# Optimization experiments

Measured on AMD Instinct MI355X. Metric: run time of the kernel, lower is better.

## Reference

```python
import jax, jax.numpy as jnp
import numpy as np

EMB = 1024
HEADS = 16
DH = EMB // HEADS
EPS = 1e-5


def _layernorm(x, w, b):
    mean = jnp.mean(x, axis=-1, keepdims=True)
    var = jnp.mean((x - mean) ** 2, axis=-1, keepdims=True)  # unbiased=False
    return w * (x - mean) / jnp.sqrt(var + EPS) + b


def _gelu_tanh(x):
    c = jnp.sqrt(jnp.asarray(2.0 / jnp.pi, x.dtype))
    return 0.5 * x * (1.0 + jnp.tanh(c * (x + 0.044715 * x ** 3)))


def setup_inputs() -> dict:
    key = jax.random.key(0)
    ks = jax.random.split(key, 8)
    B, N = 2, 2048
    s = lambda fan_in: 1.0 / np.sqrt(fan_in)
    # weights stored as [in, out] (torch Linear applied as x @ W.T == x @ W_here)
    return {
        "x": jax.random.normal(ks[0], (B, N, EMB), jnp.float32),
        "ln1_w": jnp.ones((EMB,), jnp.float32),
        "ln1_b": jnp.zeros((EMB,), jnp.float32),
        "w_qkv": jax.random.normal(ks[1], (EMB, 3 * EMB), jnp.float32) * s(EMB),  # qkv_bias=False
        "w_attn_proj": jax.random.normal(ks[2], (EMB, EMB), jnp.float32) * s(EMB),
        "b_attn_proj": jnp.zeros((EMB,), jnp.float32),
        "ln2_w": jnp.ones((EMB,), jnp.float32),
        "ln2_b": jnp.zeros((EMB,), jnp.float32),
        "w_fc": jax.random.normal(ks[3], (EMB, 4 * EMB), jnp.float32) * s(EMB),
        "b_fc": jnp.zeros((4 * EMB,), jnp.float32),
        "w_proj": jax.random.normal(ks[4], (4 * EMB, EMB), jnp.float32) * s(4 * EMB),
        "b_proj": jnp.zeros((EMB,), jnp.float32),
    }


def reference(x, ln1_w, ln1_b, w_qkv, w_attn_proj, b_attn_proj,
              ln2_w, ln2_b, w_fc, b_fc, w_proj, b_proj):
    B, N, _ = x.shape
    # --- attention sublayer (pre-LN) ---
    h = _layernorm(x, ln1_w, ln1_b)
    qkv = h @ w_qkv  # [B,N,3E]
    q, k, v = jnp.split(qkv, 3, axis=-1)
    # [B,H,N,Dh]
    q = q.reshape(B, N, HEADS, DH).transpose(0, 2, 1, 3)
    k = k.reshape(B, N, HEADS, DH).transpose(0, 2, 1, 3)
    v = v.reshape(B, N, HEADS, DH).transpose(0, 2, 1, 3)
    scores = jnp.einsum("bhqd,bhkd->bhqk", q, k) * (DH ** -0.5)
    causal = jnp.tril(jnp.ones((N, N), bool))
    scores = jnp.where(causal, scores, -jnp.inf)
    attn = jax.nn.softmax(scores, axis=-1)  # attn_pdrop=0 (eval)
    ctx = jnp.einsum("bhqk,bhkd->bhqd", attn, v)
    ctx = ctx.transpose(0, 2, 1, 3).reshape(B, N, EMB)
    x = x + (ctx @ w_attn_proj + b_attn_proj)  # resid_pdrop=0
    # --- MLP sublayer (pre-LN) ---
    h = _layernorm(x, ln2_w, ln2_b)
    h = _gelu_tanh(h @ w_fc + b_fc)
    x = x + (h @ w_proj + b_proj)
    return x
```

## Files before the change

kernel.cpp:

```cpp
#include <hip/hip_runtime.h>
#include <stdint.h>

#define EMB 1024
#define NHEAD 16
#define DH 64
#define SEQ 2048
#define NTOK 4096

typedef __attribute__((ext_vector_type(8))) short s16x8;
typedef __attribute__((ext_vector_type(4))) short s16x4;
typedef __attribute__((ext_vector_type(4))) float f32x4;
typedef __attribute__((ext_vector_type(4))) unsigned short u16x4;

__device__ __forceinline__ unsigned short f2bf(float f){
    union { float f; unsigned int u; } v; v.f = f;
    unsigned int r = v.u + 0x7fffu + ((v.u >> 16) & 1u);
    return (unsigned short)(r >> 16);
}

__device__ __forceinline__ f32x4 mfma16(s16x8 a, s16x8 b, f32x4 c){
    return __builtin_amdgcn_mfma_f32_16x16x32_bf16(a, b, c, 0, 0, 0);
}

__device__ __forceinline__ void gload16(const void* g, void* l){
    __builtin_amdgcn_global_load_lds((const __attribute__((address_space(1))) void*)g,
                                     (__attribute__((address_space(3))) void*)l, 16, 0, 0);
}

__device__ __forceinline__ s16x8 cat8(s16x4 a, s16x4 b){
    s16x8 r;
    r[0]=a[0]; r[1]=a[1]; r[2]=a[2]; r[3]=a[3];
    r[4]=b[0]; r[5]=b[1]; r[6]=b[2]; r[7]=b[3];
    return r;
}

__device__ __forceinline__ unsigned cvtpk(float lo, float hi){
    unsigned r;
    asm("v_cvt_pk_bf16_f32 %0, %1, %2" : "=v"(r) : "v"(lo), "v"(hi));
    return r;
}

__device__ __forceinline__ s16x8 qscale(s16x8 q){
    s16x8 r;
    #pragma unroll
    for (int e = 0; e < 8; ++e){
        union { float f; unsigned u; } v;
        v.u = ((unsigned)(unsigned short)q[e]) << 16;
        v.f *= 0.125f;
        r[e] = (short)f2bf(v.f);
    }
    return r;
}

__global__ __launch_bounds__(256) void convT4_kernel(const float* __restrict__ q, unsigned short* __restrict__ qo,
                                                     const float* __restrict__ a, unsigned short* __restrict__ ao,
                                                     const float* __restrict__ f, unsigned short* __restrict__ fo,
                                                     const float* __restrict__ p, unsigned short* __restrict__ po){
    __shared__ float tile[32][33];
    int id = blockIdx.x;
    const float* in; unsigned short* out; int R, C, bx, by;
    if (id < 3072)      { in = q; out = qo; R = 1024; C = 3072; bx = id % 96;  by = id / 96;  }
    else if (id < 4096) { id -= 3072; in = a; out = ao; R = 1024; C = 1024; bx = id % 32; by = id / 32; }
    else if (id < 8192) { id -= 4096; in = f; out = fo; R = 1024; C = 4096; bx = id % 128; by = id / 128; }
    else                { id -= 8192; in = p; out = po; R = 4096; C = 1024; bx = id % 32; by = id / 32; }
    const int c0 = bx * 32, r0 = by * 32;
    const int tx = threadIdx.x, ty = threadIdx.y;
    #pragma unroll
    for (int k = 0; k < 4; ++k)
        tile[ty*4+k][tx] = in[(long)(r0 + ty*4 + k) * C + c0 + tx];
    __syncthreads();
    #pragma unroll
    for (int k = 0; k < 4; ++k)
        out[(long)(c0 + ty*4 + k) * R + r0 + tx] = f2bf(tile[tx][ty*4+k]);
}

__global__ __launch_bounds__(256) void vT_kernel(const unsigned short* __restrict__ qkv,
                                                 unsigned short* __restrict__ vtg){
    __shared__ unsigned short tile[64*64];
    const int bh = blockIdx.y, b = bh >> 4, h = bh & 15;
    const int n0 = blockIdx.x * 64;
    const int t = threadIdx.x;
    const int nr = t >> 3, c0 = (t & 7) * 8;
    #pragma unroll
    for (int hh = 0; hh < 2; ++hh){
        const int n = nr + hh*32;
        uint4 vv = *(const uint4*)&qkv[(long)(b*SEQ + n0 + n)*3072 + 2048 + h*64 + c0];
        *(uint4*)((char*)tile + n*128 + ((c0*2) ^ (((n>>3)&7)<<4))) = vv;
    }
    __syncthreads();
    #pragma unroll
    for (int hh = 0; hh < 2; ++hh){
        const int d = nr + hh*32;
        union { unsigned short u[8]; uint4 v; } tmp;
        #pragma unroll
        for (int j = 0; j < 8; ++j){
            const int n = c0 + j;
            tmp.u[j] = *(const unsigned short*)((char*)tile + n*128 + ((d*2) ^ (((n>>3)&7)<<4)));
        }
        *(uint4*)&vtg[((long)bh*64 + d)*2048 + n0 + c0] = tmp.v;
    }
}

__global__ __launch_bounds__(256) void ln_kernel(const float* __restrict__ x,
                                                 const float* __restrict__ w,
                                                 const float* __restrict__ b,
                                                 unsigned short* __restrict__ out){
    const int row = blockIdx.x, tid = threadIdx.x;
    const float4 v = ((const float4*)(x + (long)row * EMB))[tid];
    float s  = v.x + v.y + v.z + v.w;
    float ss = v.x*v.x + v.y*v.y + v.z*v.z + v.w*v.w;
    #pragma unroll
    for (int off = 32; off >= 1; off >>= 1){
        s  += __shfl_xor(s,  off, 64);
        ss += __shfl_xor(ss, off, 64);
    }
    __shared__ float ps[4], pss[4];
    const int wv = tid >> 6;
    if ((tid & 63) == 0){ ps[wv] = s; pss[wv] = ss; }
    __syncthreads();
    s  = ps[0] + ps[1] + ps[2] + ps[3];
    ss = pss[0] + pss[1] + pss[2] + pss[3];
    const float mean = s * (1.0f/EMB);
    const float var  = ss * (1.0f/EMB) - mean*mean;
    const float rstd = rsqrtf(var + 1e-5f);
    const float4 wv4 = ((const float4*)w)[tid];
    const float4 bv4 = ((const float4*)b)[tid];
    u16x4 o;
    o[0] = f2bf((v.x - mean) * rstd * wv4.x + bv4.x);
    o[1] = f2bf((v.y - mean) * rstd * wv4.y + bv4.y);
    o[2] = f2bf((v.z - mean) * rstd * wv4.z + bv4.z);
    o[3] = f2bf((v.w - mean) * rstd * wv4.w + bv4.w);
    *(u16x4*)(out + (long)row * EMB + tid * 4) = o;
}

template<int EPI>
__global__ __launch_bounds__(256, 2) void gemm4_kernel(const unsigned short* __restrict__ A,
                                                       const unsigned short* __restrict__ Bt,
                                                       const float* __restrict__ bias,
                                                       void* __restrict__ out0,
                                                       int M, int N, int K,
                                                       int xr, int yr){
    __shared__ unsigned short As[2][128*64];
    __shared__ unsigned short Bs[2][128*64];
    const int tid = threadIdx.x, lane = tid & 63, w = tid >> 6;
    const int lm = lane & 15, g = lane >> 4;
    const int wr = w >> 1, wc = w & 1;

    const int gx = gridDim.x;
    const int o = blockIdx.y * gx + blockIdx.x;
    const int x = o & 7, j = o >> 3;
    const int nrx = gx / xr;
    const int m0 = ((x / nrx) * yr + j / xr) * 128;
    const int n0 = ((x % nrx) * xr + j % xr) * 128;
    const int nkt = K / 64;

    const int r8 = tid >> 3;
    const int src = (((tid & 7) * 16) ^ ((r8 & 7) << 4)) >> 1;
    char* AsB = (char*)&As[0][0];
    char* BsB = (char*)&Bs[0][0];

    auto stage = [&](int bu, int kt){
        #pragma unroll
        for (int p = 0; p < 4; ++p)
            gload16(&A[(long)(m0 + p*32 + r8) * K + kt + src], AsB + bu*16384 + p*4096 + tid*16);
        #pragma unroll
        for (int p = 0; p < 4; ++p)
            gload16(&Bt[(long)(n0 + p*32 + r8) * K + kt + src], BsB + bu*16384 + p*4096 + tid*16);
    };

    f32x4 zero = {0.0f, 0.0f, 0.0f, 0.0f};
    f32x4 acc[4][4];
    #pragma unroll
    for (int i = 0; i < 4; ++i)
        #pragma unroll
        for (int jj = 0; jj < 4; ++jj) acc[i][jj] = zero;

    stage(0, 0);
    int cur = 0;
    const int axor = (lm & 7) << 4;
    for (int t = 0; t < nkt; ++t){
        if (t + 1 < nkt){
            stage(cur ^ 1, (t + 1) * 64);
            asm volatile("s_waitcnt vmcnt(8)" ::: "memory");
        } else {
            asm volatile("s_waitcnt vmcnt(0)" ::: "memory");
        }
        __builtin_amdgcn_s_barrier();
        asm volatile("" ::: "memory");
        const char* Ab = AsB + cur*16384;
        const char* Bb = BsB + cur*16384;
        #pragma unroll
        for (int kk = 0; kk < 2; ++kk){
            s16x8 af[4], bf[4];
            #pragma unroll
            for (int i = 0; i < 4; ++i)
                af[i] = *(const s16x8*)(Ab + (wr*64 + i*16 + lm)*128 + ((kk*64 + g*16) ^ axor));
            #pragma unroll
            for (int jj = 0; jj < 4; ++jj)
                bf[jj] = *(const s16x8*)(Bb + (wc*64 + jj*16 + lm)*128 + ((kk*64 + g*16) ^ axor));
            asm volatile("s_waitcnt lgkmcnt(0)" ::: "memory");
            __builtin_amdgcn_sched_barrier(0);
            __builtin_amdgcn_s_setprio(1);
            #pragma unroll
            for (int i = 0; i < 4; ++i)
                #pragma unroll
                for (int jj = 0; jj < 4; ++jj)
                    acc[i][jj] = mfma16(bf[jj], af[i], acc[i][jj]);
            __builtin_amdgcn_s_setprio(0);
        }
        asm volatile("" ::: "memory");
        __builtin_amdgcn_s_barrier();
        asm volatile("" ::: "memory");
        cur ^= 1;
    }

    #pragma unroll
    for (int i = 0; i < 4; ++i){
        const int row = m0 + wr*64 + i*16 + lm;
        #pragma unroll
        for (int jj = 0; jj < 4; ++jj){
            const int col = n0 + wc*64 + jj*16 + 4*g;
            const f32x4 v = acc[i][jj];
            if (EPI == 0){
                u16x4 ov;
                ov[0] = f2bf(v[0]); ov[1] = f2bf(v[1]);
                ov[2] = f2bf(v[2]); ov[3] = f2bf(v[3]);
                *(u16x4*)&((unsigned short*)out0)[(long)row * N + col] = ov;
            } else {
                u16x4 ov;
                #pragma unroll
                for (int r = 0; r < 4; ++r){
                    const float xx = v[r] + bias[col + r];
                    const float z = 0.7978845608f * (xx + 0.044715f * xx * xx * xx);
                    ov[r] = f2bf(xx / (1.0f + __expf(-2.0f * z)));
                }
                *(u16x4*)&((unsigned short*)out0)[(long)row * N + col] = ov;
            }
        }
    }
}

__global__ __launch_bounds__(256, 3) void gemm5_kernel(const unsigned short* __restrict__ A,
                                                       const unsigned short* __restrict__ Bt,
                                                       const float* __restrict__ bias,
                                                       const float* __restrict__ resid,
                                                       float* __restrict__ out0,
                                                       int M, int N, int K,
                                                       int xr, int yr){
    __shared__ unsigned short As[2][128*64];
    __shared__ unsigned short Bs[2][64*64];
    const int tid = threadIdx.x, lane = tid & 63, w = tid >> 6;
    const int lm = lane & 15, g = lane >> 4;
    const int wr = w >> 1, wc = w & 1;

    const int gx = gridDim.x;
    const int o = blockIdx.y * gx + blockIdx.x;
    const int x = o & 7, j = o >> 3;
    const int nrx = gx / xr;
    const int m0 = ((x / nrx) * yr + j / xr) * 128;
    const int n0 = ((x % nrx) * xr + j % xr) * 64;
    const int nkt = K / 64;

    const int r8 = tid >> 3;
    const int src = (((tid & 7) * 16) ^ ((r8 & 7) << 4)) >> 1;
    char* AsB = (char*)&As[0][0];
    char* BsB = (char*)&Bs[0][0];

    auto stage = [&](int bu, int kt){
        #pragma unroll
        for (int p = 0; p < 4; ++p)
            gload16(&A[(long)(m0 + p*32 + r8) * K + kt + src], AsB + bu*16384 + p*4096 + tid*16);
        #pragma unroll
        for (int p = 0; p < 2; ++p)
            gload16(&Bt[(long)(n0 + p*32 + r8) * K + kt + src], BsB + bu*8192 + p*4096 + tid*16);
    };

    f32x4 zero = {0.0f, 0.0f, 0.0f, 0.0f};
    f32x4 acc[4][2];
    #pragma unroll
    for (int i = 0; i < 4; ++i)
        #pragma unroll
        for (int jj = 0; jj < 2; ++jj) acc[i][jj] = zero;

    stage(0, 0);
    int cur = 0;
    const int axor = (lm & 7) << 4;
    for (int t = 0; t < nkt; ++t){
        if (t + 1 < nkt){
            stage(cur ^ 1, (t + 1) * 64);
            asm volatile("s_waitcnt vmcnt(6)" ::: "memory");
        } else {
            asm volatile("s_waitcnt vmcnt(0)" ::: "memory");
        }
        __builtin_amdgcn_s_barrier();
        asm volatile("" ::: "memory");
        const char* Ab = AsB + cur*16384;
        const char* Bb = BsB + cur*8192;
        #pragma unroll
        for (int kk = 0; kk < 2; ++kk){
            s16x8 af[4], bf[2];
            #pragma unroll
            for (int i = 0; i < 4; ++i)
                af[i] = *(const s16x8*)(Ab + (wr*64 + i*16 + lm)*128 + ((kk*64 + g*16) ^ axor));
            #pragma unroll
            for (int jj = 0; jj < 2; ++jj)
                bf[jj] = *(const s16x8*)(Bb + (wc*32 + jj*16 + lm)*128 + ((kk*64 + g*16) ^ axor));
            asm volatile("s_waitcnt lgkmcnt(0)" ::: "memory");
            __builtin_amdgcn_sched_barrier(0);
            __builtin_amdgcn_s_setprio(1);
            #pragma unroll
            for (int i = 0; i < 4; ++i)
                #pragma unroll
                for (int jj = 0; jj < 2; ++jj)
                    acc[i][jj] = mfma16(bf[jj], af[i], acc[i][jj]);
            __builtin_amdgcn_s_setprio(0);
        }
        asm volatile("" ::: "memory");
        __builtin_amdgcn_s_barrier();
        asm volatile("" ::: "memory");
        cur ^= 1;
    }

    #pragma unroll
    for (int i = 0; i < 4; ++i){
        const int row = m0 + wr*64 + i*16 + lm;
        #pragma unroll
        for (int jj = 0; jj < 2; ++jj){
            const int col = n0 + wc*32 + jj*16 + 4*g;
            const f32x4 v = acc[i][jj];
            const float4 bb = *(const float4*)&bias[col];
            const float4 rr = *(const float4*)&resid[(long)row * N + col];
            float4 ov;
            ov.x = v[0] + bb.x + rr.x;
            ov.y = v[1] + bb.y + rr.y;
            ov.z = v[2] + bb.z + rr.z;
            ov.w = v[3] + bb.w + rr.w;
            *(float4*)&out0[(long)row * N + col] = ov;
        }
    }
}

__global__ __launch_bounds__(256) void attn_kernel(const unsigned short* __restrict__ qkv,
                                                   const unsigned short* __restrict__ vtg,
                                                   unsigned short* __restrict__ ctx){
    __shared__ unsigned short Ks[3][4096];
    __shared__ unsigned short Vs[3][4096];
    int id0 = blockIdx.y * 16 + blockIdx.x;
    const int id = (id0 & 7) * 64 + (id0 >> 3);
    const int pair = id & 15, bh = id >> 4;
    const int b = bh >> 4, h = bh & 15;
    const int tid = threadIdx.x, lane = tid & 63, w = tid >> 6;
    const int lm = lane & 15, g = lane >> 4;
    const long qkvb = (long)b * SEQ * 3072;
    const unsigned short* kglob = qkv + qkvb + 1024 + h*64;
    const unsigned short* vglob = vtg + (long)bh * 64 * 2048;

    const int srow = tid >> 3;
    const int soff = (tid & 7) * 16;
    const int swz = (lm & 7) << 4;
    f32x4 zero = {0.0f, 0.0f, 0.0f, 0.0f};

    #pragma unroll 1
    for (int grp = 0; grp < 2; ++grp){
        const int qg = (grp == 0) ? pair : (31 - pair);
        const int q0 = qg * 64;
        const int nt = qg + 1;
        const int qrow = q0 + w*16 + lm;

        const unsigned short* qrp = qkv + qkvb + (long)qrow*3072 + h*64;
        const s16x8 qf0 = qscale(*(const s16x8*)(qrp + g*8));
        const s16x8 qf1 = qscale(*(const s16x8*)(qrp + 32 + g*8));

        f32x4 o[4];
        #pragma unroll
        for (int d = 0; d < 4; ++d) o[d] = zero;
        float lsum = 0.0f;

        auto stageKV = [&](int t, int bu){
            const int kv0 = t * 64;
            #pragma unroll
            for (int hh = 0; hh < 2; ++hh){
                const int row = srow + hh*32;
                const int sw  = soff ^ ((row & 7) << 4);
                gload16(kglob + (long)(kv0 + row)*3072 + (sw >> 1),
                        (char*)&Ks[bu][0] + hh*4096 + w*1024);
                gload16(vglob + (long)row*2048 + kv0 + (sw >> 1),
                        (char*)&Vs[bu][0] + hh*4096 + w*1024);
            }
        };
        auto qkt = [&](int bu, f32x4* sc){
            const char* Kb = (const char*)&Ks[bu][0];
            #pragma unroll
            for (int s = 0; s < 4; ++s){
                const char* rp = Kb + (s*16 + lm)*128;
                s16x8 kf0 = *(const s16x8*)(rp + ((g*16) ^ swz));
                s16x8 kf1 = *(const s16x8*)(rp + ((64 + g*16) ^ swz));
                f32x4 a = mfma16(kf0, qf0, zero);
                sc[s] = mfma16(kf1, qf1, a);
            }
        };

        __builtin_amdgcn_s_barrier();
        asm volatile("" ::: "memory");
        stageKV(0, 0);
        if (nt > 1){
            stageKV(1, 1);
            asm volatile("s_waitcnt vmcnt(4)" ::: "memory");
        } else {
            asm volatile("s_waitcnt vmcnt(0)" ::: "memory");
        }
        __builtin_amdgcn_s_barrier();
        asm volatile("" ::: "memory");

        f32x4 sc[4], scN[4];
        qkt(0, sc);

        #pragma unroll 1
        for (int t = 0; t < nt; ++t){
            const bool more = (t + 1 < nt);
            if (more){
                asm volatile("s_waitcnt vmcnt(0)" ::: "memory");
                __builtin_amdgcn_s_barrier();
                asm volatile("" ::: "memory");
                if (t + 2 < nt) stageKV(t + 2, (t + 2) % 3);
                qkt((t + 1) % 3, scN);
            }

            if (t == nt - 1){
                #pragma unroll
                for (int s = 0; s < 4; ++s)
                    #pragma unroll
                    for (int r = 0; r < 4; ++r)
                        if (s*16 + 4*g + r > w*16 + lm) sc[s][r] = -1e30f;
            }
            float pp[4][4];
            #pragma unroll
            for (int s = 0; s < 4; ++s)
                #pragma unroll
                for (int r = 0; r < 4; ++r){
                    const float e = __expf(sc[s][r]);
                    pp[s][r] = e;
                    lsum += e;
                }

            union { unsigned u[4]; s16x8 v; } P0, P1;
            P0.u[0] = cvtpk(pp[0][0], pp[0][1]);
            P0.u[1] = cvtpk(pp[0][2], pp[0][3]);
            P0.u[2] = cvtpk(pp[1][0], pp[1][1]);
            P0.u[3] = cvtpk(pp[1][2], pp[1][3]);
            P1.u[0] = cvtpk(pp[2][0], pp[2][1]);
            P1.u[1] = cvtpk(pp[2][2], pp[2][3]);
            P1.u[2] = cvtpk(pp[3][0], pp[3][1]);
            P1.u[3] = cvtpk(pp[3][2], pp[3][3]);

            const char* Vb = (const char*)&Vs[t % 3][0];
            #pragma unroll
            for (int d = 0; d < 4; ++d){
                const char* vrp = Vb + (d*16 + lm)*128;
                s16x4 a0 = *(const s16x4*)(vrp + ((g*8) ^ swz));
                s16x4 a1 = *(const s16x4*)(vrp + ((32 + g*8) ^ swz));
                o[d] = mfma16(cat8(a0, a1), P0.v, o[d]);
                s16x4 b0 = *(const s16x4*)(vrp + ((64 + g*8) ^ swz));
                s16x4 b1 = *(const s16x4*)(vrp + ((96 + g*8) ^ swz));
                o[d] = mfma16(cat8(b0, b1), P1.v, o[d]);
            }
            if (more){
                #pragma unroll
                for (int s4 = 0; s4 < 4; ++s4) sc[s4] = scN[s4];
            }
        }

        lsum += __shfl_xor(lsum, 16, 64);
        lsum += __shfl_xor(lsum, 32, 64);
        const float inv = 1.0f / lsum;
        unsigned short* cw = ctx + (long)(b*SEQ + qrow)*EMB + h*DH + 4*g;
        #pragma unroll
        for (int d = 0; d < 4; ++d){
            u16x4 ov;
            ov[0] = f2bf(o[d][0]*inv); ov[1] = f2bf(o[d][1]*inv);
            ov[2] = f2bf(o[d][2]*inv); ov[3] = f2bf(o[d][3]*inv);
            *(u16x4*)(cw + d*16) = ov;
        }
    }
}

extern "C" void kernel_launch(void* const* d_in, const int* in_sizes, int n_in,
                              void* d_out, int out_size, void* d_ws, size_t ws_size,
                              hipStream_t stream){
    const float* x     = (const float*)d_in[0];
    const float* ln1_w = (const float*)d_in[1];
    const float* ln1_b = (const float*)d_in[2];
    const float* w_qkv = (const float*)d_in[3];
    const float* w_ap  = (const float*)d_in[4];
    const float* b_ap  = (const float*)d_in[5];
    const float* ln2_w = (const float*)d_in[6];
    const float* ln2_b = (const float*)d_in[7];
    const float* w_fc  = (const float*)d_in[8];
    const float* b_fc  = (const float*)d_in[9];
    const float* w_pr  = (const float*)d_in[10];
    const float* b_pr  = (const float*)d_in[11];
    float* out = (float*)d_out;

    char* ws = (char*)d_ws;
    unsigned short* wqkvT = (unsigned short*)(ws + 0);
    unsigned short* wapT  = (unsigned short*)(ws + 6291456);
    unsigned short* wfcT  = (unsigned short*)(ws + 8388608);
    unsigned short* wprT  = (unsigned short*)(ws + 16777216);
    unsigned short* h1    = (unsigned short*)(ws + 25165824);
    unsigned short* vtg   = (unsigned short*)(ws + 25165824);
    unsigned short* qkv   = (unsigned short*)(ws + 33554432);
    unsigned short* ctx   = (unsigned short*)(ws + 58720256);
    float*          x1    = (float*)(ws + 67108864);
    unsigned short* h2    = (unsigned short*)(ws + 83886080);
    unsigned short* afc   = (unsigned short*)(ws + 92274688);

    convT4_kernel<<<12288, dim3(32, 8, 1), 0, stream>>>(
        w_qkv, wqkvT, w_ap, wapT, w_fc, wfcT, w_pr, wprT);

    ln_kernel<<<NTOK, 256, 0, stream>>>(x, ln1_w, ln1_b, h1);

    gemm4_kernel<0><<<dim3(3072/128, NTOK/128), 256, 0, stream>>>(
        h1, wqkvT, nullptr, qkv, NTOK, 3072, 1024, 12, 8);

    vT_kernel<<<dim3(SEQ/64, 32), 256, 0, stream>>>(qkv, vtg);

    attn_kernel<<<dim3(16, 32), 256, 0, stream>>>(qkv, vtg, ctx);

    gemm5_kernel<<<dim3(1024/64, NTOK/128), 256, 0, stream>>>(
        ctx, wapT, b_ap, x, x1, NTOK, 1024, 1024, 8, 8);

    ln_kernel<<<NTOK, 256, 0, stream>>>(x1, ln2_w, ln2_b, h2);

    gemm4_kernel<2><<<dim3(4096/128, NTOK/128), 256, 0, stream>>>(
        h2, wfcT, b_fc, afc, NTOK, 4096, 1024, 16, 8);

    gemm5_kernel<<<dim3(1024/64, NTOK/128), 256, 0, stream>>>(
        afc, wprT, b_pr, x1, out, NTOK, 1024, 4096, 8, 8);
}
```

Baseline: 238.6 us.

## Replace block-tiled GEMMs with single-wave 64x64 tile GEMM kernel

Replaces the 256-thread, 128x128 and 128x64 tile GEMM kernels with one templated kernel in which a single 64-lane wavefront owns a 64x64 output tile, using a K-step of 32 and no block barriers. All four projection GEMMs now launch many small one-wave blocks, and the bias-plus-residual epilogue is folded into the same template. The intent is to remove barrier synchronisation and gain more resident waves and finer scheduling. In exchange, each wave re-reads A and B tiles with much less reuse, which raises global and L2 traffic per FLOP. It also drops the priority hints around the MFMA block.

```diff
diff --git a/kernel.cpp b/kernel.cpp
--- a/kernel.cpp
+++ b/kernel.cpp
@@ -134,38 +134,39 @@
 }
 
 template<int EPI>
-__global__ __launch_bounds__(256, 2) void gemm4_kernel(const unsigned short* __restrict__ A,
-                                                       const unsigned short* __restrict__ Bt,
-                                                       const float* __restrict__ bias,
-                                                       void* __restrict__ out0,
-                                                       int M, int N, int K,
-                                                       int xr, int yr){
-    __shared__ unsigned short As[2][128*64];
-    __shared__ unsigned short Bs[2][128*64];
-    const int tid = threadIdx.x, lane = tid & 63, w = tid >> 6;
+__global__ __launch_bounds__(64, 3) void gemm6_kernel(const unsigned short* __restrict__ A,
+                                                      const unsigned short* __restrict__ Bt,
+                                                      const float* __restrict__ bias,
+                                                      const float* __restrict__ resid,
+                                                      void* __restrict__ out0,
+                                                      int M, int N, int K,
+                                                      int xr, int yr){
+    __shared__ unsigned short As[2][2048];
+    __shared__ unsigned short Bs[2][2048];
+    const int lane = threadIdx.x;
     const int lm = lane & 15, g = lane >> 4;
-    const int wr = w >> 1, wc = w & 1;
-
-    const int gx = gridDim.x;
-    const int o = blockIdx.y * gx + blockIdx.x;
+
+    const int gx = N >> 6;
+    const int o = blockIdx.x;
     const int x = o & 7, j = o >> 3;
     const int nrx = gx / xr;
-    const int m0 = ((x / nrx) * yr + j / xr) * 128;
-    const int n0 = ((x % nrx) * xr + j % xr) * 128;
-    const int nkt = K / 64;
-
-    const int r8 = tid >> 3;
-    const int src = (((tid & 7) * 16) ^ ((r8 & 7) << 4)) >> 1;
-    char* AsB = (char*)&As[0][0];
-    char* BsB = (char*)&Bs[0][0];
+    const int m0 = ((x / nrx) * yr + j / xr) * 64;
+    const int n0 = ((x % nrx) * xr + j % xr) * 64;
+    const int nkt = K >> 5;
+
+    const int srow = lane >> 2;
+    const int srcoff = ((lane & 3) * 8) ^ ((srow & 3) << 3);
+    const unsigned short* Ab = A + (long)(m0 + srow) * K + srcoff;
+    const unsigned short* Bb = Bt + (long)(n0 + srow) * K + srcoff;
+    const long rstep = (long)16 * K;
 
     auto stage = [&](int bu, int kt){
         #pragma unroll
         for (int p = 0; p < 4; ++p)
-            gload16(&A[(long)(m0 + p*32 + r8) * K + kt + src], AsB + bu*16384 + p*4096 + tid*16);
+            gload16(Ab + p*rstep + kt, (char*)&As[bu][0] + p*1024 + lane*16);
         #pragma unroll
         for (int p = 0; p < 4; ++p)
-            gload16(&Bt[(long)(n0 + p*32 + r8) * K + kt + src], BsB + bu*16384 + p*4096 + tid*16);
+            gload16(Bb + p*rstep + kt, (char*)&Bs[bu][0] + p*1024 + lane*16);
     };
 
     f32x4 zero = {0.0f, 0.0f, 0.0f, 0.0f};
@@ -176,166 +177,64 @@
         for (int jj = 0; jj < 4; ++jj) acc[i][jj] = zero;
 
     stage(0, 0);
-    int cur = 0;
-    const int axor = (lm & 7) << 4;
+    const int rxor = (lm & 3) << 4;
     for (int t = 0; t < nkt; ++t){
         if (t + 1 < nkt){
-            stage(cur ^ 1, (t + 1) * 64);
+            stage((t + 1) & 1, (t + 1) * 32);
             asm volatile("s_waitcnt vmcnt(8)" ::: "memory");
         } else {
             asm volatile("s_waitcnt vmcnt(0)" ::: "memory");
         }
-        __builtin_amdgcn_s_barrier();
-        asm volatile("" ::: "memory");
-        const char* Ab = AsB + cur*16384;
-        const char* Bb = BsB + cur*16384;
-        #pragma unroll
-        for (int kk = 0; kk < 2; ++kk){
-            s16x8 af[4], bf[4];
-            #pragma unroll
-            for (int i = 0; i < 4; ++i)
-                af[i] = *(const s16x8*)(Ab + (wr*64 + i*16 + lm)*128 + ((kk*64 + g*16) ^ axor));
+        const char* Ap = (const char*)&As[t & 1][0];
+        const char* Bp = (const char*)&Bs[t & 1][0];
+        s16x8 af[4], bf[4];
+        #pragma unroll
+        for (int i = 0; i < 4; ++i)
+            af[i] = *(const s16x8*)(Ap + (i*16 + lm)*64 + ((g*16) ^ rxor));
+        #pragma unroll
+        for (int jj = 0; jj < 4; ++jj)
+            bf[jj] = *(const s16x8*)(Bp + (jj*16 + lm)*64 + ((g*16) ^ rxor));
+        asm volatile("s_waitcnt lgkmcnt(0)" ::: "memory");
+        __builtin_amdgcn_sched_barrier(0);
+        #pragma unroll
+        for (int i = 0; i < 4; ++i)
             #pragma unroll
             for (int jj = 0; jj < 4; ++jj)
-                bf[jj] = *(const s16x8*)(Bb + (wc*64 + jj*16 + lm)*128 + ((kk*64 + g*16) ^ axor));
-            asm volatile("s_waitcnt lgkmcnt(0)" ::: "memory");
-            __builtin_amdgcn_sched_barrier(0);
-            __builtin_amdgcn_s_setprio(1);
-            #pragma unroll
-            for (int i = 0; i < 4; ++i)
-                #pragma unroll
-                for (int jj = 0; jj < 4; ++jj)
-                    acc[i][jj] = mfma16(bf[jj], af[i], acc[i][jj]);
-            __builtin_amdgcn_s_setprio(0);
-        }
-        asm volatile("" ::: "memory");
-        __builtin_amdgcn_s_barrier();
-        asm volatile("" ::: "memory");
-        cur ^= 1;
+                acc[i][jj] = mfma16(bf[jj], af[i], acc[i][jj]);
     }
 
     #pragma unroll
     for (int i = 0; i < 4; ++i){
-        const int row = m0 + wr*64 + i*16 + lm;
+        const int row = m0 + i*16 + lm;
         #pragma unroll
         for (int jj = 0; jj < 4; ++jj){
-            const int col = n0 + wc*64 + jj*16 + 4*g;
+            const int col = n0 + jj*16 + 4*g;
             const f32x4 v = acc[i][jj];
             if (EPI == 0){
                 u16x4 ov;
                 ov[0] = f2bf(v[0]); ov[1] = f2bf(v[1]);
                 ov[2] = f2bf(v[2]); ov[3] = f2bf(v[3]);
                 *(u16x4*)&((unsigned short*)out0)[(long)row * N + col] = ov;
+            } else if (EPI == 1){
+                const float4 bb = *(const float4*)&bias[col];
+                const float4 rr = *(const float4*)&resid[(long)row * N + col];
+                float4 ov;
+                ov.x = v[0] + bb.x + rr.x;
+                ov.y = v[1] + bb.y + rr.y;
+                ov.z = v[2] + bb.z + rr.z;
+                ov.w = v[3] + bb.w + rr.w;
+                *(float4*)&((float*)out0)[(long)row * N + col] = ov;
             } else {
+                const float4 bb = *(const float4*)&bias[col];
                 u16x4 ov;
                 #pragma unroll
                 for (int r = 0; r < 4; ++r){
-                    const float xx = v[r] + bias[col + r];
+                    const float xx = v[r] + ((const float*)&bb)[r];
                     const float z = 0.7978845608f * (xx + 0.044715f * xx * xx * xx);
                     ov[r] = f2bf(xx / (1.0f + __expf(-2.0f * z)));
                 }
                 *(u16x4*)&((unsigned short*)out0)[(long)row * N + col] = ov;
             }
-        }
-    }
-}
-
-__global__ __launch_bounds__(256, 3) void gemm5_kernel(const unsigned short* __restrict__ A,
-                                                       const unsigned short* __restrict__ Bt,
-                                                       const float* __restrict__ bias,
-                                                       const float* __restrict__ resid,
-                                                       float* __restrict__ out0,
-                                                       int M, int N, int K,
-                                                       int xr, int yr){
-    __shared__ unsigned short As[2][128*64];
-    __shared__ unsigned short Bs[2][64*64];
-    const int tid = threadIdx.x, lane = tid & 63, w = tid >> 6;
-    const int lm = lane & 15, g = lane >> 4;
-    const int wr = w >> 1, wc = w & 1;
-
-    const int gx = gridDim.x;
-    const int o = blockIdx.y * gx + blockIdx.x;
-    const int x = o & 7, j = o >> 3;
-    const int nrx = gx / xr;
-    const int m0 = ((x / nrx) * yr + j / xr) * 128;
-    const int n0 = ((x % nrx) * xr + j % xr) * 64;
-    const int nkt = K / 64;
-
-    const int r8 = tid >> 3;
-    const int src = (((tid & 7) * 16) ^ ((r8 & 7) << 4)) >> 1;
-    char* AsB = (char*)&As[0][0];
-    char* BsB = (char*)&Bs[0][0];
-
-    auto stage = [&](int bu, int kt){
-        #pragma unroll
-        for (int p = 0; p < 4; ++p)
-            gload16(&A[(long)(m0 + p*32 + r8) * K + kt + src], AsB + bu*16384 + p*4096 + tid*16);
-        #pragma unroll
-        for (int p = 0; p < 2; ++p)
-            gload16(&Bt[(long)(n0 + p*32 + r8) * K + kt + src], BsB + bu*8192 + p*4096 + tid*16);
-    };
-
-    f32x4 zero = {0.0f, 0.0f, 0.0f, 0.0f};
-    f32x4 acc[4][2];
-    #pragma unroll
-    for (int i = 0; i < 4; ++i)
-        #pragma unroll
-        for (int jj = 0; jj < 2; ++jj) acc[i][jj] = zero;
-
-    stage(0, 0);
-    int cur = 0;
-    const int axor = (lm & 7) << 4;
-    for (int t = 0; t < nkt; ++t){
-        if (t + 1 < nkt){
-            stage(cur ^ 1, (t + 1) * 64);
-            asm volatile("s_waitcnt vmcnt(6)" ::: "memory");
-        } else {
-            asm volatile("s_waitcnt vmcnt(0)" ::: "memory");
-        }
-        __builtin_amdgcn_s_barrier();
-        asm volatile("" ::: "memory");
-        const char* Ab = AsB + cur*16384;
-        const char* Bb = BsB + cur*8192;
-        #pragma unroll
-        for (int kk = 0; kk < 2; ++kk){
-            s16x8 af[4], bf[2];
-            #pragma unroll
-            for (int i = 0; i < 4; ++i)
-                af[i] = *(const s16x8*)(Ab + (wr*64 + i*16 + lm)*128 + ((kk*64 + g*16) ^ axor));
-            #pragma unroll
-            for (int jj = 0; jj < 2; ++jj)
-                bf[jj] = *(const s16x8*)(Bb + (wc*32 + jj*16 + lm)*128 + ((kk*64 + g*16) ^ axor));
-            asm volatile("s_waitcnt lgkmcnt(0)" ::: "memory");
-            __builtin_amdgcn_sched_barrier(0);
-            __builtin_amdgcn_s_setprio(1);
-            #pragma unroll
-            for (int i = 0; i < 4; ++i)
-                #pragma unroll
-                for (int jj = 0; jj < 2; ++jj)
-                    acc[i][jj] = mfma16(bf[jj], af[i], acc[i][jj]);
-            __builtin_amdgcn_s_setprio(0);
-        }
-        asm volatile("" ::: "memory");
-        __builtin_amdgcn_s_barrier();
-        asm volatile("" ::: "memory");
-        cur ^= 1;
-    }
-
-    #pragma unroll
-    for (int i = 0; i < 4; ++i){
-        const int row = m0 + wr*64 + i*16 + lm;
-        #pragma unroll
-        for (int jj = 0; jj < 2; ++jj){
-            const int col = n0 + wc*32 + jj*16 + 4*g;
-            const f32x4 v = acc[i][jj];
-            const float4 bb = *(const float4*)&bias[col];
-            const float4 rr = *(const float4*)&resid[(long)row * N + col];
-            float4 ov;
-            ov.x = v[0] + bb.x + rr.x;
-            ov.y = v[1] + bb.y + rr.y;
-            ov.z = v[2] + bb.z + rr.z;
-            ov.w = v[3] + bb.w + rr.w;
-            *(float4*)&out0[(long)row * N + col] = ov;
         }
     }
 }
@@ -519,21 +418,21 @@
 
     ln_kernel<<<NTOK, 256, 0, stream>>>(x, ln1_w, ln1_b, h1);
 
-    gemm4_kernel<0><<<dim3(3072/128, NTOK/128), 256, 0, stream>>>(
-        h1, wqkvT, nullptr, qkv, NTOK, 3072, 1024, 12, 8);
+    gemm6_kernel<0><<<3072, 64, 0, stream>>>(
+        h1, wqkvT, nullptr, nullptr, qkv, NTOK, 3072, 1024, 24, 16);
 
     vT_kernel<<<dim3(SEQ/64, 32), 256, 0, stream>>>(qkv, vtg);
 
     attn_kernel<<<dim3(16, 32), 256, 0, stream>>>(qkv, vtg, ctx);
 
-    gemm5_kernel<<<dim3(1024/64, NTOK/128), 256, 0, stream>>>(
-        ctx, wapT, b_ap, x, x1, NTOK, 1024, 1024, 8, 8);
+    gemm6_kernel<1><<<1024, 64, 0, stream>>>(
+        ctx, wapT, b_ap, x, x1, NTOK, 1024, 1024, 8, 16);
 
     ln_kernel<<<NTOK, 256, 0, stream>>>(x1, ln2_w, ln2_b, h2);
 
-    gemm4_kernel<2><<<dim3(4096/128, NTOK/128), 256, 0, stream>>>(
-        h2, wfcT, b_fc, afc, NTOK, 4096, 1024, 16, 8);
-
-    gemm5_kernel<<<dim3(1024/64, NTOK/128), 256, 0, stream>>>(
-        afc, wprT, b_pr, x1, out, NTOK, 1024, 4096, 8, 8);
-}
+    gemm6_kernel<2><<<4096, 64, 0, stream>>>(
+        h2, wfcT, b_fc, nullptr, afc, NTOK, 4096, 1024, 32, 16);
+
+    gemm6_kernel<1><<<1024, 64, 0, stream>>>(
+        afc, wprT, b_pr, x1, out, NTOK, 1024, 4096, 8, 16);
+}
```

Measured after the change: 300.1 us. 25.8% more time.

## Shrink GEMM K-tile to 32 for higher occupancy and swap attn-proj GEMM kernel

Applied to the files above, without the earlier changes.

The QKV and FC GEMMs now stage 32-wide K tiles instead of 64, which halves shared memory per block. The launch bound rises to 4 blocks per CU and the XOR swizzle is reworked to match the narrower rows. The attention output projection moves from gemm5 to a new generic templated GEMM (128x64 tile, 2x2 waves) that has a simple double buffer, no swizzle and scalar epilogue stores. The higher occupancy is meant to hide latency, at the cost of twice as many barriers per K and possible LDS bank conflicts in the new unswizzled kernel.

```diff
diff --git a/kernel.cpp b/kernel.cpp
--- a/kernel.cpp
+++ b/kernel.cpp
@@ -134,14 +134,14 @@
 }
 
 template<int EPI>
-__global__ __launch_bounds__(256, 2) void gemm4_kernel(const unsigned short* __restrict__ A,
+__global__ __launch_bounds__(256, 4) void gemm7_kernel(const unsigned short* __restrict__ A,
                                                        const unsigned short* __restrict__ Bt,
                                                        const float* __restrict__ bias,
                                                        void* __restrict__ out0,
                                                        int M, int N, int K,
                                                        int xr, int yr){
-    __shared__ unsigned short As[2][128*64];
-    __shared__ unsigned short Bs[2][128*64];
+    __shared__ unsigned short As[2][128*32];
+    __shared__ unsigned short Bs[2][128*32];
     const int tid = threadIdx.x, lane = tid & 63, w = tid >> 6;
     const int lm = lane & 15, g = lane >> 4;
     const int wr = w >> 1, wc = w & 1;
@@ -152,20 +152,22 @@
     const int nrx = gx / xr;
     const int m0 = ((x / nrx) * yr + j / xr) * 128;
     const int n0 = ((x % nrx) * xr + j % xr) * 128;
-    const int nkt = K / 64;
-
-    const int r8 = tid >> 3;
-    const int src = (((tid & 7) * 16) ^ ((r8 & 7) << 4)) >> 1;
+    const int nkt = K >> 5;
+
+    const int srow = tid >> 2;
+    const int srcoff = (((tid & 3) ^ ((srow >> 1) & 3)) << 3);
+    const unsigned short* Ap0 = A + (long)(m0 + srow) * K + srcoff;
+    const unsigned short* Bp0 = Bt + (long)(n0 + srow) * K + srcoff;
     char* AsB = (char*)&As[0][0];
     char* BsB = (char*)&Bs[0][0];
 
     auto stage = [&](int bu, int kt){
         #pragma unroll
-        for (int p = 0; p < 4; ++p)
-            gload16(&A[(long)(m0 + p*32 + r8) * K + kt + src], AsB + bu*16384 + p*4096 + tid*16);
-        #pragma unroll
-        for (int p = 0; p < 4; ++p)
-            gload16(&Bt[(long)(n0 + p*32 + r8) * K + kt + src], BsB + bu*16384 + p*4096 + tid*16);
+        for (int p = 0; p < 2; ++p)
+            gload16(Ap0 + (long)p*64*K + kt, AsB + bu*8192 + p*4096 + tid*16);
+        #pragma unroll
+        for (int p = 0; p < 2; ++p)
+            gload16(Bp0 + (long)p*64*K + kt, BsB + bu*8192 + p*4096 + tid*16);
     };
 
     f32x4 zero = {0.0f, 0.0f, 0.0f, 0.0f};
@@ -177,37 +179,34 @@
 
     stage(0, 0);
     int cur = 0;
-    const int axor = (lm & 7) << 4;
+    const int rsw = ((lm >> 1) & 3) << 4;
     for (int t = 0; t < nkt; ++t){
         if (t + 1 < nkt){
-            stage(cur ^ 1, (t + 1) * 64);
-            asm volatile("s_waitcnt vmcnt(8)" ::: "memory");
+            stage(cur ^ 1, (t + 1) * 32);
+            asm volatile("s_waitcnt vmcnt(4)" ::: "memory");
         } else {
             asm volatile("s_waitcnt vmcnt(0)" ::: "memory");
         }
         __builtin_amdgcn_s_barrier();
         asm volatile("" ::: "memory");
-        const char* Ab = AsB + cur*16384;
-        const char* Bb = BsB + cur*16384;
-        #pragma unroll
-        for (int kk = 0; kk < 2; ++kk){
-            s16x8 af[4], bf[4];
-            #pragma unroll
-            for (int i = 0; i < 4; ++i)
-                af[i] = *(const s16x8*)(Ab + (wr*64 + i*16 + lm)*128 + ((kk*64 + g*16) ^ axor));
+        const char* Ab = AsB + cur*8192;
+        const char* Bb = BsB + cur*8192;
+        s16x8 af[4], bf[4];
+        #pragma unroll
+        for (int i = 0; i < 4; ++i)
+            af[i] = *(const s16x8*)(Ab + (wr*64 + i*16 + lm)*64 + ((g*16) ^ rsw));
+        #pragma unroll
+        for (int jj = 0; jj < 4; ++jj)
+            bf[jj] = *(const s16x8*)(Bb + (wc*64 + jj*16 + lm)*64 + ((g*16) ^ rsw));
+        asm volatile("s_waitcnt lgkmcnt(0)" ::: "memory");
+        __builtin_amdgcn_sched_barrier(0);
+        __builtin_amdgcn_s_setprio(1);
+        #pragma unroll
+        for (int i = 0; i < 4; ++i)
             #pragma unroll
             for (int jj = 0; jj < 4; ++jj)
-                bf[jj] = *(const s16x8*)(Bb + (wc*64 + jj*16 + lm)*128 + ((kk*64 + g*16) ^ axor));
-            asm volatile("s_waitcnt lgkmcnt(0)" ::: "memory");
-            __builtin_amdgcn_sched_barrier(0);
-            __builtin_amdgcn_s_setprio(1);
-            #pragma unroll
-            for (int i = 0; i < 4; ++i)
-                #pragma unroll
-                for (int jj = 0; jj < 4; ++jj)
-                    acc[i][jj] = mfma16(bf[jj], af[i], acc[i][jj]);
-            __builtin_amdgcn_s_setprio(0);
-        }
+                acc[i][jj] = mfma16(bf[jj], af[i], acc[i][jj]);
+        __builtin_amdgcn_s_setprio(0);
         asm volatile("" ::: "memory");
         __builtin_amdgcn_s_barrier();
         asm volatile("" ::: "memory");
@@ -340,6 +339,89 @@
     }
 }
 
+template<int EPI, int BM, int BN, int WR, int WC>
+__global__ __launch_bounds__(WR*WC*64) void gemm_kernel(const unsigned short* __restrict__ A,
+                                                        const unsigned short* __restrict__ Bt,
+                                                        const float* __restrict__ bias,
+                                                        const float* __restrict__ resid,
+                                                        void* __restrict__ out0,
+                                                        int M, int N, int K){
+    constexpr int NW = WR * WC;
+    constexpr int NT = NW * 64;
+    constexpr int FI = BM / (WR * 16);
+    constexpr int FJ = BN / (WC * 16);
+    __shared__ unsigned short As[2][BM * 32];
+    __shared__ unsigned short Bs[2][BN * 32];
+    const int tid  = threadIdx.x;
+    const int lane = tid & 63, w = tid >> 6;
+    const int lm = lane & 15, g = lane >> 4;
+    const int wr = w / WC, wc = w % WC;
+
+    const int gx = gridDim.x;
+    const int nwg = gx * gridDim.y;
+    int id = blockIdx.y * gx + blockIdx.x;
+    id = (id & 7) * (nwg >> 3) + (id >> 3);
+    const int m0 = (id / gx) * BM, n0 = (id % gx) * BN;
+
+    f32x4 zero = {0.0f, 0.0f, 0.0f, 0.0f};
+    f32x4 acc[FI][FJ];
+    #pragma unroll
+    for (int i = 0; i < FI; ++i)
+        #pragma unroll
+        for (int j = 0; j < FJ; ++j) acc[i][j] = zero;
+
+    auto stage = [&](int kt, int bu){
+        #pragma unroll
+        for (int p = 0; p < BM/(NT/4); ++p)
+            gload16(&A[(long)(m0 + p*(NT/4) + (tid>>2)) * K + kt + (tid&3)*8],
+                    (char*)&As[bu][0] + p*(NT*16) + tid*16);
+        #pragma unroll
+        for (int p = 0; p < BN/(NT/4); ++p)
+            gload16(&Bt[(long)(n0 + p*(NT/4) + (tid>>2)) * K + kt + (tid&3)*8],
+                    (char*)&Bs[bu][0] + p*(NT*16) + tid*16);
+    };
+
+    stage(0, 0);
+    int cur = 0;
+    const int nkt = K / 32;
+    for (int t = 0; t < nkt; ++t){
+        __syncthreads();
+        if (t + 1 < nkt) stage((t+1)*32, cur ^ 1);
+        s16x8 af[FI], bf[FJ];
+        #pragma unroll
+        for (int i = 0; i < FI; ++i)
+            af[i] = *(const s16x8*)&As[cur][(wr*(FI*16) + i*16 + lm)*32 + g*8];
+        #pragma unroll
+        for (int j = 0; j < FJ; ++j)
+            bf[j] = *(const s16x8*)&Bs[cur][(wc*(FJ*16) + j*16 + lm)*32 + g*8];
+        #pragma unroll
+        for (int i = 0; i < FI; ++i)
+            #pragma unroll
+            for (int j = 0; j < FJ; ++j)
+                acc[i][j] = mfma16(af[i], bf[j], acc[i][j]);
+        cur ^= 1;
+    }
+
+    #pragma unroll
+    for (int i = 0; i < FI; ++i){
+        #pragma unroll
+        for (int r = 0; r < 4; ++r){
+            const int row = m0 + wr*(FI*16) + i*16 + 4*g + r;
+            #pragma unroll
+            for (int j = 0; j < FJ; ++j){
+                const int col = n0 + wc*(FJ*16) + j*16 + lm;
+                const float v = acc[i][j][r];
+                if (EPI == 1){
+                    ((float*)out0)[(long)row * N + col] =
+                        v + bias[col] + resid[(long)row * N + col];
+                } else {
+                    ((unsigned short*)out0)[(long)row * N + col] = f2bf(v);
+                }
+            }
+        }
+    }
+}
+
 __global__ __launch_bounds__(256) void attn_kernel(const unsigned short* __restrict__ qkv,
                                                    const unsigned short* __restrict__ vtg,
                                                    unsigned short* __restrict__ ctx){
@@ -519,19 +601,19 @@
 
     ln_kernel<<<NTOK, 256, 0, stream>>>(x, ln1_w, ln1_b, h1);
 
-    gemm4_kernel<0><<<dim3(3072/128, NTOK/128), 256, 0, stream>>>(
+    gemm7_kernel<0><<<dim3(3072/128, NTOK/128), 256, 0, stream>>>(
         h1, wqkvT, nullptr, qkv, NTOK, 3072, 1024, 12, 8);
 
     vT_kernel<<<dim3(SEQ/64, 32), 256, 0, stream>>>(qkv, vtg);
 
     attn_kernel<<<dim3(16, 32), 256, 0, stream>>>(qkv, vtg, ctx);
 
-    gemm5_kernel<<<dim3(1024/64, NTOK/128), 256, 0, stream>>>(
-        ctx, wapT, b_ap, x, x1, NTOK, 1024, 1024, 8, 8);
+    gemm_kernel<1,128,64,2,2><<<dim3(1024/64, NTOK/128), 256, 0, stream>>>(
+        ctx, wapT, b_ap, x, x1, NTOK, 1024, 1024);
 
     ln_kernel<<<NTOK, 256, 0, stream>>>(x1, ln2_w, ln2_b, h2);
 
-    gemm4_kernel<2><<<dim3(4096/128, NTOK/128), 256, 0, stream>>>(
+    gemm7_kernel<2><<<dim3(4096/128, NTOK/128), 256, 0, stream>>>(
         h2, wfcT, b_fc, afc, NTOK, 4096, 1024, 16, 8);
 
     gemm5_kernel<<<dim3(1024/64, NTOK/128), 256, 0, stream>>>(
```

After: 239.1 us. Within noise of the previous version (+0.2%).
